# Optimization experiments

Measured on AMD Instinct MI355X. Metric: run time of the kernel, lower is better.

Reference implementation:

```python
import jax, jax.numpy as jnp
import numpy as np

EMBED_DIM = 1024
N_HEADS = 16
DK = EMBED_DIM // N_HEADS


def setup_inputs() -> dict:
    key = jax.random.key(0)
    ks = jax.random.split(key, 9)
    s = 1.0 / np.sqrt(EMBED_DIM)
    d = EMBED_DIM
    return {
        "x": jax.random.normal(ks[0], (2, 2048, d), dtype=jnp.float32),
        "Wq": jax.random.uniform(ks[1], (d, d), jnp.float32, -s, s),
        "bq": jax.random.uniform(ks[2], (d,), jnp.float32, -s, s),
        "Wk": jax.random.uniform(ks[3], (d, d), jnp.float32, -s, s),
        "bk": jax.random.uniform(ks[4], (d,), jnp.float32, -s, s),
        "Wv": jax.random.uniform(ks[5], (d, d), jnp.float32, -s, s),
        "bv": jax.random.uniform(ks[6], (d,), jnp.float32, -s, s),
        "Wo": jax.random.uniform(ks[7], (d, d), jnp.float32, -s, s),
        "bo": jax.random.uniform(ks[8], (d,), jnp.float32, -s, s),
    }


def reference(x, Wq, bq, Wk, bk, Wv, bv, Wo, bo):
    B, S, D = x.shape
    H, dk = N_HEADS, DK
    # QKV projections
    q = (x @ Wq + bq).reshape(B, S, H, dk).transpose(0, 2, 1, 3)  # [B,H,S,dk]
    k = (x @ Wk + bk).reshape(B, S, H, dk).transpose(0, 2, 1, 3)
    v = (x @ Wv + bv).reshape(B, S, H, dk).transpose(0, 2, 1, 3)
    # scaled dot-product attention with full score matrix (faithful to source)
    scores = jnp.einsum("bhqd,bhkd->bhqk", q, k) / jnp.sqrt(jnp.float32(dk))
    attn = jax.nn.softmax(scores, axis=-1)
    out = jnp.einsum("bhqk,bhkd->bhqd", attn, v)  # [B,H,S,dk]
    out = out.transpose(0, 2, 1, 3).reshape(B, S, D)
    return out @ Wo + bo
```

## Files before the change

kernel.cpp:

```cpp
#include <hip/hip_runtime.h>

typedef unsigned short u16;
typedef unsigned int u32;
typedef __attribute__((ext_vector_type(8))) short short8;
typedef __attribute__((ext_vector_type(4))) float float4v;
typedef __attribute__((ext_vector_type(4))) unsigned int uint4v;

struct alignas(8) U16x4 { u16 x, y, z, w; };

__device__ __forceinline__ u16 f2b(float f) {
    union { float f; unsigned int u; } v; v.f = f;
    unsigned int r = (v.u >> 16) & 1u;
    v.u += 0x7fffu + r;
    return (u16)(v.u >> 16);
}

__device__ __forceinline__ float b2f(u16 u) {
    union { unsigned int u; float f; } v; v.u = ((u32)u) << 16; return v.f;
}

__device__ __forceinline__ u32 cvt_pk_bf16(float lo, float hi) {
    u32 d;
    asm("v_cvt_pk_bf16_f32 %0, %1, %2" : "=v"(d) : "v"(lo), "v"(hi));
    return d;
}

__device__ __forceinline__ void gld16(const u16* g, u16* l) {
    __builtin_amdgcn_global_load_lds(
        (const __attribute__((address_space(1))) void*)g,
        (__attribute__((address_space(3))) void*)l, 16, 0, 0);
}

__device__ __forceinline__ short8 frag8(const u16* base, int row, int cg) {
    return *(const short8*)(base + row * 64 + ((cg ^ (row & 7)) << 3));
}

__global__ __launch_bounds__(256) void prep_kernel(
    const float* __restrict__ x, const float* __restrict__ W0,
    const float* __restrict__ W1, const float* __restrict__ W2,
    const float* __restrict__ W3, u16* __restrict__ xb,
    u16* __restrict__ T0, u16* __restrict__ T1,
    u16* __restrict__ T2, u16* __restrict__ T3) {
    __shared__ float tile[32][33];
    int id = blockIdx.x;
    if (id < 4096) {
        size_t i = ((size_t)id * 256 + threadIdx.x) * 4;
        float4 v = *(const float4*)(x + i);
        U16x4 o;
        o.x = f2b(v.x); o.y = f2b(v.y); o.z = f2b(v.z); o.w = f2b(v.w);
        *(U16x4*)(xb + i) = o;
        return;
    }
    int r = id - 4096;
    int z = r >> 10, tl = r & 1023;
    const float* W = (z == 0) ? W0 : (z == 1) ? W1 : (z == 2) ? W2 : W3;
    u16* T = (z == 0) ? T0 : (z == 1) ? T1 : (z == 2) ? T2 : T3;
    int t = threadIdx.x;
    int tx = t & 31, ty = t >> 5;
    int bn = (tl & 31) * 32, bk = (tl >> 5) * 32;
#pragma unroll
    for (int p = 0; p < 4; ++p) {
        int k = ty + p * 8;
        tile[k][tx] = W[(size_t)(bk + k) * 1024 + bn + tx];
    }
    __syncthreads();
#pragma unroll
    for (int p = 0; p < 4; ++p) {
        int n = ty + p * 8;
        T[(size_t)(bn + n) * 1024 + bk + tx] = f2b(tile[tx][n]);
    }
}

__global__ __launch_bounds__(512, 4) void qkv_kernel(
    const u16* __restrict__ X,
    const u16* __restrict__ WqT, const u16* __restrict__ WkT, const u16* __restrict__ WvT,
    const float* __restrict__ bq, const float* __restrict__ bk, const float* __restrict__ bv,
    u16* __restrict__ Qo, u16* __restrict__ Ko, u16* __restrict__ VTo) {
    __shared__ __align__(16) u16 As[64 * 64];
    __shared__ __align__(16) u16 Bs[3][128 * 64];
    int id = blockIdx.x;
    int m = (id & 7) | (((id >> 3) & 7) << 3);
    int n = id >> 6;
    int t = threadIdx.x;
    int m0 = m * 64, n0 = n * 128;
    int lane = t & 63, wid = t >> 6;
    int l16 = lane & 15, quad = lane >> 4;
    int rl = lane >> 3, cs = lane & 7;

    int z_st = (wid - 2) >> 1, half = wid & 1;
    const u16* gsrcB = (z_st == 0) ? WqT : (z_st == 1) ? WkT : WvT;

    float4v acc[3][4];
    float4v zero4 = {0.f, 0.f, 0.f, 0.f};
#pragma unroll
    for (int z = 0; z < 3; ++z)
#pragma unroll
        for (int i = 0; i < 4; ++i) acc[z][i] = zero4;

    for (int k0 = 0; k0 < 1024; k0 += 64) {
        __syncthreads();
        if (wid < 2) {
#pragma unroll
            for (int p = 0; p < 4; ++p) {
                int q = wid * 4 + p;
                int row = q * 8 + rl;
                int c = cs ^ (row & 7);
                gld16(X + (size_t)(m0 + row) * 1024 + k0 + c * 8, As + q * 512);
            }
        } else {
#pragma unroll
            for (int p = 0; p < 8; ++p) {
                int q = half * 8 + p;
                int row = q * 8 + rl;
                int c = cs ^ (row & 7);
                gld16(gsrcB + (size_t)(n0 + row) * 1024 + k0 + c * 8,
                      &Bs[z_st][0] + q * 512);
            }
        }
        __syncthreads();
#pragma unroll
        for (int ks = 0; ks < 64; ks += 32) {
            int cg = (ks >> 3) + quad;
            short8 af[4];
#pragma unroll
            for (int i = 0; i < 4; ++i)
                af[i] = frag8(As, i * 16 + l16, cg);
#pragma unroll
            for (int z = 0; z < 3; ++z) {
                short8 bf = frag8(&Bs[z][0], wid * 16 + l16, cg);
#pragma unroll
                for (int i = 0; i < 4; ++i)
                    acc[z][i] = __builtin_amdgcn_mfma_f32_16x16x32_bf16(
                        af[i], bf, acc[z][i], 0, 0, 0);
            }
        }
    }

    const float QSCALE = 0.18033688011112042f;
    int n1 = n0 + wid * 16 + l16;
    float bql = bq[n1], bkl = bk[n1], bvl = bv[n1];
#pragma unroll
    for (int i = 0; i < 4; ++i) {
        int mbase = m0 + i * 16 + quad * 4;
#pragma unroll
        for (int r = 0; r < 4; ++r) {
            Qo[(size_t)(mbase + r) * 1024 + n1] =
                f2b((acc[0][i][r] + bql) * QSCALE);
            Ko[(size_t)(mbase + r) * 1024 + n1] =
                f2b(acc[1][i][r] + bkl);
        }
        int bidx = mbase >> 11, s = mbase & 2047;
        size_t base =
            ((size_t)((bidx * 16 + (n1 >> 6)) * 64 + (n1 & 63))) * 2048 + s;
        U16x4 pk;
        pk.x = f2b(acc[2][i][0] + bvl);
        pk.y = f2b(acc[2][i][1] + bvl);
        pk.z = f2b(acc[2][i][2] + bvl);
        pk.w = f2b(acc[2][i][3] + bvl);
        *(U16x4*)(VTo + base) = pk;
    }
}

__global__ __launch_bounds__(256, 4) void oproj_kernel(const u16* __restrict__ X,
                                                       const u16* __restrict__ WoT,
                                                       const float* __restrict__ bias,
                                                       float* __restrict__ out) {
    __shared__ __align__(16) u16 As[64 * 64];
    __shared__ __align__(16) u16 Bs[64 * 64];
    int id = blockIdx.x;
    int m = (id & 7) | (((id >> 3) & 7) << 3);
    int n = id >> 6;
    int t = threadIdx.x;
    int m0 = m * 64, n0 = n * 64;
    int lane = t & 63, wid = t >> 6;
    int l16 = lane & 15, quad = lane >> 4;
    int rl = lane >> 3, cs = lane & 7;

    float4v acc[4];
    float4v zero4 = {0.f, 0.f, 0.f, 0.f};
#pragma unroll
    for (int i = 0; i < 4; ++i) acc[i] = zero4;

    for (int k0 = 0; k0 < 1024; k0 += 64) {
        __syncthreads();
#pragma unroll
        for (int p = 0; p < 2; ++p) {
            int blk = wid * 2 + p;
            int row = blk * 8 + rl;
            int c = cs ^ (row & 7);
            gld16(X + (size_t)(m0 + row) * 1024 + k0 + c * 8, As + blk * 512);
            gld16(WoT + (size_t)(n0 + row) * 1024 + k0 + c * 8, Bs + blk * 512);
        }
        __syncthreads();
#pragma unroll
        for (int ks = 0; ks < 64; ks += 32) {
            int cg = (ks >> 3) + quad;
            short8 af[4];
#pragma unroll
            for (int i = 0; i < 4; ++i) af[i] = frag8(As, i * 16 + l16, cg);
            short8 bf = frag8(Bs, wid * 16 + l16, cg);
#pragma unroll
            for (int i = 0; i < 4; ++i)
                acc[i] = __builtin_amdgcn_mfma_f32_16x16x32_bf16(
                    af[i], bf, acc[i], 0, 0, 0);
        }
    }

    int n1 = n0 + wid * 16 + l16;
    float bvl = bias[n1];
#pragma unroll
    for (int i = 0; i < 4; ++i) {
        int mbase = m0 + i * 16 + quad * 4;
#pragma unroll
        for (int r = 0; r < 4; ++r)
            out[(size_t)(mbase + r) * 1024 + n1] = acc[i][r] + bvl;
    }
}

__global__ __launch_bounds__(256, 4) void flash_kernel(const u16* __restrict__ Q,
                                                       const u16* __restrict__ Kn,
                                                       const u16* __restrict__ VT,
                                                       u16* __restrict__ Opart,
                                                       float* __restrict__ lpart) {
    __shared__ __align__(16) u16 Ks[2][64 * 64];
    __shared__ __align__(16) u16 Vs[2][64 * 64];

    int id = blockIdx.x;
    int bh = (id & 7) | (((id >> 3) & 3) << 3);
    int rest = id >> 5;
    int qb = rest & 15, kvz = rest >> 4;
    int b = bh >> 4, h = bh & 15;
    int t = threadIdx.x;
    int wid = t >> 6, lane = t & 63;
    int l16 = lane & 15, quad = lane >> 4;
    int rl = lane >> 3, cs = lane & 7;
    int q0 = qb * 128 + wid * 32;
    size_t kbase = (size_t)(b * 2048) * 1024 + h * 64;
    size_t vbase = (size_t)(bh * 64) * 2048;
    int kv0 = kvz * 1024;

    short8 qf[2][2];
#pragma unroll
    for (int j = 0; j < 2; ++j)
#pragma unroll
        for (int kk = 0; kk < 2; ++kk)
            qf[j][kk] = *(const short8*)(
                Q + ((size_t)(b * 2048 + q0 + j * 16 + l16)) * 1024 + h * 64 +
                kk * 32 + quad * 8);

    float4v oacc[2][4];
    float4v den[2];
    float4v zero4 = {0.f, 0.f, 0.f, 0.f};
    const short8 ones8 = {(short)0x3F80, (short)0x3F80, (short)0x3F80, (short)0x3F80,
                          (short)0x3F80, (short)0x3F80, (short)0x3F80, (short)0x3F80};
#pragma unroll
    for (int ip = 0; ip < 2; ++ip) {
        den[ip] = zero4;
#pragma unroll
        for (int jd = 0; jd < 4; ++jd) oacc[ip][jd] = zero4;
    }

#define STAGE_KV(buf, kv)                                                     \
    {                                                                         \
        _Pragma("unroll") for (int p2 = 0; p2 < 2; ++p2) {                    \
            int p = wid * 2 + p2;                                             \
            int row = p * 8 + rl;                                             \
            int c = cs ^ (row & 7);                                           \
            int key = (((row >> 4) & 1) << 5) | (((row >> 2) & 3) << 3) |     \
                      (((row >> 5) & 1) << 2) | (row & 3);                    \
            gld16(Kn + kbase + (size_t)((kv) + key) * 1024 + c * 8,           \
                  &Ks[buf][p * 512]);                                         \
            gld16(VT + vbase + (size_t)row * 2048 + (kv) + c * 8,             \
                  &Vs[buf][p * 512]);                                         \
        }                                                                     \
    }

    STAGE_KV(0, kv0);

    for (int kvi = 0; kvi < 16; ++kvi) {
        int buf = kvi & 1;
        __syncthreads();
        if (kvi + 1 < 16) STAGE_KV(buf ^ 1, kv0 + (kvi + 1) * 64);

        u32 pw[2][4][2];
#pragma unroll
        for (int i = 0; i < 4; ++i) {
            float4v s0 = zero4, s1 = zero4;
            __builtin_amdgcn_s_setprio(1);
#pragma unroll
            for (int kk = 0; kk < 2; ++kk) {
                short8 kf = frag8(&Ks[buf][0], i * 16 + l16, kk * 4 + quad);
                s0 = __builtin_amdgcn_mfma_f32_16x16x32_bf16(kf, qf[0][kk], s0, 0, 0, 0);
                s1 = __builtin_amdgcn_mfma_f32_16x16x32_bf16(kf, qf[1][kk], s1, 0, 0, 0);
            }
            __builtin_amdgcn_s_setprio(0);
#pragma unroll
            for (int j = 0; j < 2; ++j) {
                float4v s = (j == 0) ? s0 : s1;
                float e0f = __builtin_amdgcn_exp2f(s[0]);
                float e1f = __builtin_amdgcn_exp2f(s[1]);
                float e2f = __builtin_amdgcn_exp2f(s[2]);
                float e3f = __builtin_amdgcn_exp2f(s[3]);
                pw[j][i][0] = cvt_pk_bf16(e0f, e1f);
                pw[j][i][1] = cvt_pk_bf16(e2f, e3f);
            }
        }

        __builtin_amdgcn_s_setprio(1);
#pragma unroll
        for (int kk = 0; kk < 2; ++kk) {
            int cg = kk * 4 + quad;
            short8 vf[4];
#pragma unroll
            for (int jd = 0; jd < 4; ++jd)
                vf[jd] = frag8(&Vs[buf][0], jd * 16 + l16, cg);
#pragma unroll
            for (int j = 0; j < 2; ++j) {
                union { uint4v u; short8 s; } pu;
                pu.u = (uint4v){pw[j][kk][0], pw[j][kk][1],
                                pw[j][2 + kk][0], pw[j][2 + kk][1]};
#pragma unroll
                for (int jd = 0; jd < 4; ++jd)
                    oacc[j][jd] = __builtin_amdgcn_mfma_f32_16x16x32_bf16(
                        pu.s, vf[jd], oacc[j][jd], 0, 0, 0);
                den[j] = __builtin_amdgcn_mfma_f32_16x16x32_bf16(
                    pu.s, ones8, den[j], 0, 0, 0);
            }
        }
        __builtin_amdgcn_s_setprio(0);
    }
#undef STAGE_KV

    size_t obase = (size_t)kvz * 4194304;
#pragma unroll
    for (int ip = 0; ip < 2; ++ip)
#pragma unroll
        for (int r = 0; r < 4; ++r) {
            int q = q0 + ip * 16 + quad * 4 + r;
#pragma unroll
            for (int jd = 0; jd < 4; ++jd)
                Opart[obase + ((size_t)(b * 2048 + q)) * 1024 + h * 64 +
                      jd * 16 + l16] = f2b(oacc[ip][jd][r]);
        }
    if (l16 == 0) {
#pragma unroll
        for (int j = 0; j < 2; ++j)
#pragma unroll
            for (int r = 0; r < 4; ++r) {
                int q = q0 + j * 16 + quad * 4 + r;
                lpart[kvz * 65536 + (b * 2048 + q) * 16 + h] = den[j][r];
            }
    }
}

__global__ __launch_bounds__(256) void combine_kernel(const u16* __restrict__ Op,
                                                      const float* __restrict__ lp,
                                                      u16* __restrict__ out) {
    int idx = blockIdx.x * 256 + threadIdx.x;
    size_t i = (size_t)idx * 4;
    int qg = idx >> 8;
    int d = (idx & 255) * 4;
    int h = d >> 6;
    float l0 = lp[qg * 16 + h], l1 = lp[65536 + qg * 16 + h];
    float inv = 1.0f / (l0 + l1);
    U16x4 o0 = *(const U16x4*)(Op + i);
    U16x4 o1 = *(const U16x4*)(Op + 4194304 + i);
    U16x4 o;
    o.x = f2b((b2f(o0.x) + b2f(o1.x)) * inv);
    o.y = f2b((b2f(o0.y) + b2f(o1.y)) * inv);
    o.z = f2b((b2f(o0.z) + b2f(o1.z)) * inv);
    o.w = f2b((b2f(o0.w) + b2f(o1.w)) * inv);
    *(U16x4*)(out + i) = o;
}

extern "C" void kernel_launch(void* const* d_in, const int* in_sizes, int n_in,
                              void* d_out, int out_size, void* d_ws, size_t ws_size,
                              hipStream_t stream) {
    const float* x  = (const float*)d_in[0];
    const float* Wq = (const float*)d_in[1];
    const float* bq = (const float*)d_in[2];
    const float* Wk = (const float*)d_in[3];
    const float* bk = (const float*)d_in[4];
    const float* Wv = (const float*)d_in[5];
    const float* bv = (const float*)d_in[6];
    const float* Wo = (const float*)d_in[7];
    const float* bo = (const float*)d_in[8];
    float* out = (float*)d_out;

    char* ws = (char*)d_ws;
    const size_t MB = 1024 * 1024;
    u16* xb  = (u16*)(ws);
    u16* wqt = (u16*)(ws + 8 * MB);
    u16* wkt = (u16*)(ws + 10 * MB);
    u16* wvt = (u16*)(ws + 12 * MB);
    u16* wot = (u16*)(ws + 14 * MB);
    u16* qb_ = (u16*)(ws + 16 * MB);
    u16* kb_ = (u16*)(ws + 24 * MB);
    u16* vt_ = (u16*)(ws + 32 * MB);
    u16* ab_ = (u16*)(ws + 40 * MB);
    u16* op_ = (u16*)(ws + 48 * MB);
    float* lp_ = (float*)(ws + 64 * MB);

    prep_kernel<<<8192, 256, 0, stream>>>(x, Wq, Wk, Wv, Wo, xb,
                                          wqt, wkt, wvt, wot);
    qkv_kernel<<<512, 512, 0, stream>>>(xb, wqt, wkt, wvt, bq, bk, bv,
                                        qb_, kb_, vt_);
    flash_kernel<<<1024, 256, 0, stream>>>(qb_, kb_, vt_, op_, lp_);
    combine_kernel<<<4096, 256, 0, stream>>>(op_, lp_, ab_);
    oproj_kernel<<<1024, 256, 0, stream>>>(ab_, wot, bo, out);
}
```

Baseline: 177.4 us.

## Fuse split-KV combine into output projection A-tile load

Removes the separate combine kernel and merges the two split-KV partial outputs inside the output-projection GEMM while loading the A tile. Each block precomputes per-row, per-head inverse denominators into shared memory. It then reads both partials with direct vector loads, sums and scales them, and writes bf16 into the swizzled LDS tile. This saves one launch and a full write and read of the combined activation buffer. The cost is that each partial tile is re-read by every N-column block (16 times) and the A path loses its asynchronous global-to-LDS load.

```diff
diff --git a/kernel.cpp b/kernel.cpp
--- a/kernel.cpp
+++ b/kernel.cpp
@@ -161,12 +161,14 @@
     }
 }
 
-__global__ __launch_bounds__(256, 4) void oproj_kernel(const u16* __restrict__ X,
+__global__ __launch_bounds__(256, 4) void oproj_kernel(const u16* __restrict__ Op,
+                                                       const float* __restrict__ lp,
                                                        const u16* __restrict__ WoT,
                                                        const float* __restrict__ bias,
                                                        float* __restrict__ out) {
     __shared__ __align__(16) u16 As[64 * 64];
     __shared__ __align__(16) u16 Bs[64 * 64];
+    __shared__ float invs[64][16];
     int id = blockIdx.x;
     int m = (id & 7) | (((id >> 3) & 7) << 3);
     int n = id >> 6;
@@ -176,6 +178,13 @@
     int l16 = lane & 15, quad = lane >> 4;
     int rl = lane >> 3, cs = lane & 7;
 
+#pragma unroll
+    for (int e = t; e < 1024; e += 256) {
+        int row = e >> 4, h = e & 15;
+        int qg = (m0 + row) * 16 + h;
+        invs[row][h] = 1.0f / (lp[qg] + lp[65536 + qg]);
+    }
+
     float4v acc[4];
     float4v zero4 = {0.f, 0.f, 0.f, 0.f};
 #pragma unroll
@@ -188,8 +197,25 @@
             int blk = wid * 2 + p;
             int row = blk * 8 + rl;
             int c = cs ^ (row & 7);
-            gld16(X + (size_t)(m0 + row) * 1024 + k0 + c * 8, As + blk * 512);
             gld16(WoT + (size_t)(n0 + row) * 1024 + k0 + c * 8, Bs + blk * 512);
+        }
+        int h = k0 >> 6;
+#pragma unroll
+        for (int p = 0; p < 2; ++p) {
+            int blk = wid * 2 + p;
+            int row = blk * 8 + rl;
+            size_t goff = (size_t)(m0 + row) * 1024 + k0 + cs * 8;
+            short8 o0 = *(const short8*)(Op + goff);
+            short8 o1 = *(const short8*)(Op + 4194304 + goff);
+            float iv = invs[row][h];
+            uint4v w;
+#pragma unroll
+            for (int q2 = 0; q2 < 4; ++q2) {
+                float a = (b2f((u16)o0[q2 * 2]) + b2f((u16)o1[q2 * 2])) * iv;
+                float bb = (b2f((u16)o0[q2 * 2 + 1]) + b2f((u16)o1[q2 * 2 + 1])) * iv;
+                w[q2] = cvt_pk_bf16(a, bb);
+            }
+            *(uint4v*)(As + row * 64 + ((cs ^ (row & 7)) << 3)) = w;
         }
         __syncthreads();
 #pragma unroll
@@ -353,26 +379,6 @@
     }
 }
 
-__global__ __launch_bounds__(256) void combine_kernel(const u16* __restrict__ Op,
-                                                      const float* __restrict__ lp,
-                                                      u16* __restrict__ out) {
-    int idx = blockIdx.x * 256 + threadIdx.x;
-    size_t i = (size_t)idx * 4;
-    int qg = idx >> 8;
-    int d = (idx & 255) * 4;
-    int h = d >> 6;
-    float l0 = lp[qg * 16 + h], l1 = lp[65536 + qg * 16 + h];
-    float inv = 1.0f / (l0 + l1);
-    U16x4 o0 = *(const U16x4*)(Op + i);
-    U16x4 o1 = *(const U16x4*)(Op + 4194304 + i);
-    U16x4 o;
-    o.x = f2b((b2f(o0.x) + b2f(o1.x)) * inv);
-    o.y = f2b((b2f(o0.y) + b2f(o1.y)) * inv);
-    o.z = f2b((b2f(o0.z) + b2f(o1.z)) * inv);
-    o.w = f2b((b2f(o0.w) + b2f(o1.w)) * inv);
-    *(U16x4*)(out + i) = o;
-}
-
 extern "C" void kernel_launch(void* const* d_in, const int* in_sizes, int n_in,
                               void* d_out, int out_size, void* d_ws, size_t ws_size,
                               hipStream_t stream) {
@@ -397,7 +403,6 @@
     u16* qb_ = (u16*)(ws + 16 * MB);
     u16* kb_ = (u16*)(ws + 24 * MB);
     u16* vt_ = (u16*)(ws + 32 * MB);
-    u16* ab_ = (u16*)(ws + 40 * MB);
     u16* op_ = (u16*)(ws + 48 * MB);
     float* lp_ = (float*)(ws + 64 * MB);
 
@@ -406,6 +411,5 @@
     qkv_kernel<<<512, 512, 0, stream>>>(xb, wqt, wkt, wvt, bq, bk, bv,
                                         qb_, kb_, vt_);
     flash_kernel<<<1024, 256, 0, stream>>>(qb_, kb_, vt_, op_, lp_);
-    combine_kernel<<<4096, 256, 0, stream>>>(op_, lp_, ab_);
-    oproj_kernel<<<1024, 256, 0, stream>>>(ab_, wot, bo, out);
-}
+    oproj_kernel<<<1024, 256, 0, stream>>>(op_, lp_, wot, bo, out);
+}
```

Result: no change. 178.3 us (median of 3 runs) (+0.5%).
